# Performance work log

Measured on AMD Instinct MI355X. Metric: run time of the kernel, lower is better.

## Reference

```python
import jax, jax.numpy as jnp
import numpy as np

B, S, H, MI, E, K, SI = 4, 1024, 1024, 512, 16, 2, 2048


def setup_inputs() -> dict:
    key = jax.random.key(0)
    ks = jax.random.split(key, 8)
    s = 0.02  # weight scale ~ glorot-ish
    return {
        "hidden_states": jax.random.normal(ks[0], (B, S, H), jnp.float32),
        "router_w": jax.random.normal(ks[1], (H, E), jnp.float32) * s,
        "expert_gate_up_w": jax.random.normal(ks[2], (E, H, 2 * MI), jnp.float32) * s,
        "expert_down_w": jax.random.normal(ks[3], (E, MI, H), jnp.float32) * s,
        "shared_gate_w": jax.random.normal(ks[4], (H, SI), jnp.float32) * s,
        "shared_up_w": jax.random.normal(ks[5], (H, SI), jnp.float32) * s,
        "shared_down_w": jax.random.normal(ks[6], (SI, H), jnp.float32) * s,
        "shared_expert_gate_w": jax.random.normal(ks[7], (H, 1), jnp.float32) * s,
    }


def reference(hidden_states, router_w, expert_gate_up_w, expert_down_w,
              shared_gate_w, shared_up_w, shared_down_w, shared_expert_gate_w):
    b, s, h = hidden_states.shape
    x = hidden_states.reshape(-1, h)  # [T, H]
    T = x.shape[0]

    # Shared expert: SwiGLU MLP gated by sigmoid(shared_expert_gate)
    g = jax.nn.silu(x @ shared_gate_w)          # [T, SI]
    u = x @ shared_up_w                          # [T, SI]
    shared_out = (u * g) @ shared_down_w         # [T, H]
    shared_out = jax.nn.sigmoid(x @ shared_expert_gate_w) * shared_out

    # Router: softmax -> top-k -> renormalize -> dense [T, E] routing weights
    router_logits = x @ router_w                 # [T, E]
    probs = jax.nn.softmax(router_logits, axis=-1)
    top_p, top_i = jax.lax.top_k(probs, K)       # [T, K]
    top_p = top_p / jnp.sum(top_p, axis=-1, keepdims=True)
    routing = jnp.zeros((T, probs.shape[-1]), x.dtype).at[
        jnp.arange(T)[:, None], top_i].add(top_p)  # [T, E]

    # All-experts SwiGLU (compute-all-then-select, as in source)
    gate_up = jnp.einsum('th,ehm->etm', x, expert_gate_up_w)  # [E, T, 2*MI]
    gate, up = jnp.split(gate_up, 2, axis=-1)
    hidden = up * jax.nn.silu(gate)                            # [E, T, MI]
    expert_out = jnp.einsum('eti,eih->eth', hidden, expert_down_w)  # [E, T, H]
    contrib = jnp.einsum('eth,te->th', expert_out, routing)    # [T, H]

    out = (contrib + shared_out).reshape(b, s, h)
    return out, router_logits
```

## Files before the change

kernel.cpp:

```cpp
#include <hip/hip_runtime.h>
#include <hip/hip_bf16.h>
#include <cstdint>

#define T_  4096
#define H_  1024
#define E_  16
#define MI_ 512
#define SI_ 2048
#define TK_ 8192

typedef __bf16 bf16;
typedef bf16  bf16x8 __attribute__((ext_vector_type(8)));
typedef bf16  bf16x4 __attribute__((ext_vector_type(4)));
typedef float f32x4  __attribute__((ext_vector_type(4)));

__device__ __forceinline__ void gload16(const bf16* g, bf16* lds) {
    __builtin_amdgcn_global_load_lds(
        (const __attribute__((address_space(1))) void*)(uintptr_t)(const void*)g,
        (__attribute__((address_space(3))) void*)(uintptr_t)(void*)lds,
        16, 0, 0);
}

__global__ void k_transpose_all(
    const float* __restrict__ wgu, const float* __restrict__ wdn,
    const float* __restrict__ wsg, const float* __restrict__ wsu, const float* __restrict__ wsd,
    bf16* __restrict__ ogu, bf16* __restrict__ odn,
    bf16* __restrict__ osg, bf16* __restrict__ osu, bf16* __restrict__ osd)
{
    __shared__ float tile[32][33];
    int id = blockIdx.x;
    const float* src; bf16* dst; int R, C, bx, by;
    if (id < 16384) {
        int s = id >> 10, r = id & 1023;
        src = wgu + (size_t)s * 1048576; dst = ogu + (size_t)s * 1048576;
        R = 1024; C = 1024; bx = r & 31; by = r >> 5;
    } else if (id < 24576) {
        int k = id - 16384; int s = k >> 9, r = k & 511;
        src = wdn + (size_t)s * 524288; dst = odn + (size_t)s * 524288;
        R = 512; C = 1024; bx = r & 31; by = r >> 5;
    } else if (id < 26624) {
        int r = id - 24576;
        src = wsg; dst = osg; R = 1024; C = 2048; bx = r & 63; by = r >> 6;
    } else if (id < 28672) {
        int r = id - 26624;
        src = wsu; dst = osu; R = 1024; C = 2048; bx = r & 63; by = r >> 6;
    } else {
        int r = id - 28672;
        src = wsd; dst = osd; R = 2048; C = 1024; bx = r & 31; by = r >> 5;
    }
    int c = bx * 32 + threadIdx.x;
    #pragma unroll
    for (int i = 0; i < 4; i++) {
        int r_ = by * 32 + threadIdx.y + i * 8;
        tile[threadIdx.y + i * 8][threadIdx.x] = src[(size_t)r_ * C + c];
    }
    __syncthreads();
    int rr = by * 32 + threadIdx.x;
    #pragma unroll
    for (int i = 0; i < 4; i++) {
        int cc = bx * 32 + threadIdx.y + i * 8;
        dst[(size_t)cc * R + rr] = (bf16)tile[threadIdx.x][threadIdx.y + i * 8];
    }
}

__global__ __launch_bounds__(256) void k_router(
    const float* __restrict__ x, const float* __restrict__ rw,
    const float* __restrict__ segw, float* __restrict__ logits_out,
    int* __restrict__ top_i, float* __restrict__ top_w,
    float* __restrict__ gate_scalar, bf16* __restrict__ xb)
{
    int wid = threadIdx.x >> 6, lane = threadIdx.x & 63;
    int t = blockIdx.x * 4 + wid;
    const float* xr = x + (size_t)t * H_;
    bf16* xbr = xb + (size_t)t * H_;
    float acc[E_];
    #pragma unroll
    for (int e = 0; e < E_; e++) acc[e] = 0.f;
    float accg = 0.f;
    for (int j = 0; j < H_ / 64; j++) {
        int h = j * 64 + lane;
        float xv = xr[h];
        xbr[h] = (bf16)xv;
        const float4* wrow = reinterpret_cast<const float4*>(rw + (size_t)h * E_);
        #pragma unroll
        for (int q = 0; q < 4; q++) {
            float4 w4 = wrow[q];
            acc[q*4+0] += xv * w4.x; acc[q*4+1] += xv * w4.y;
            acc[q*4+2] += xv * w4.z; acc[q*4+3] += xv * w4.w;
        }
        accg += xv * segw[h];
    }
    #pragma unroll
    for (int off = 32; off >= 1; off >>= 1) {
        #pragma unroll
        for (int e = 0; e < E_; e++) acc[e] += __shfl_xor(acc[e], off);
        accg += __shfl_xor(accg, off);
    }
    if (lane == 0) {
        float* lo = logits_out + (size_t)t * E_;
        #pragma unroll
        for (int e = 0; e < E_; e++) lo[e] = acc[e];
        int i0 = 0; float l0 = acc[0];
        #pragma unroll
        for (int e = 1; e < E_; e++) if (acc[e] > l0) { l0 = acc[e]; i0 = e; }
        int i1 = -1; float l1 = -1e30f;
        #pragma unroll
        for (int e = 0; e < E_; e++) if (e != i0 && acc[e] > l1) { l1 = acc[e]; i1 = e; }
        float w0 = 1.f / (1.f + expf(l1 - l0));
        top_i[t*2] = i0; top_i[t*2+1] = i1;
        top_w[t*2] = w0; top_w[t*2+1] = 1.f - w0;
        gate_scalar[t] = 1.f / (1.f + expf(-accg));
    }
}

__global__ __launch_bounds__(256) void k_count(const int* __restrict__ top_i, int* __restrict__ offsets) {
    __shared__ int hist[256][17];
    int tid = threadIdx.x;
    #pragma unroll
    for (int e = 0; e < E_; e++) hist[tid][e] = 0;
    __syncthreads();
    const int* mine = top_i + tid * 32;
    #pragma unroll
    for (int j = 0; j < 32; j++) hist[tid][mine[j]]++;
    __syncthreads();
    if (tid < E_) {
        int s = 0;
        for (int r = 0; r < 256; r++) s += hist[r][tid];
        hist[0][tid] = s;
    }
    __syncthreads();
    if (tid == 0) {
        int s = 0;
        for (int e = 0; e < E_; e++) { offsets[e] = s; s += hist[0][e]; }
        offsets[E_] = s;
    }
}

__global__ __launch_bounds__(256) void k_fillscan(
    const int* __restrict__ top_i, const int* __restrict__ offsets,
    int* __restrict__ slot_token, int* __restrict__ slot_pos)
{
    int e = blockIdx.x;
    int tid = threadIdx.x;
    int lane = tid & 63, w = tid >> 6;
    __shared__ int wsum[4];

    int t0 = tid * 16;
    unsigned f0 = 0, f1 = 0;
    int c = 0;
    #pragma unroll
    for (int j = 0; j < 16; j++) {
        int t = t0 + j;
        int a = top_i[t*2], b = top_i[t*2+1];
        if (a == e)      { f0 |= 1u << j; c++; }
        else if (b == e) { f1 |= 1u << j; c++; }
    }
    int incl = c;
    #pragma unroll
    for (int off = 1; off < 64; off <<= 1) {
        int v = __shfl_up(incl, off);
        if (lane >= off) incl += v;
    }
    if (lane == 63) wsum[w] = incl;
    __syncthreads();
    int wbase = 0;
    for (int i = 0; i < w; i++) wbase += wsum[i];
    int pos = offsets[e] + wbase + (incl - c);
    #pragma unroll
    for (int j = 0; j < 16; j++) {
        int t = t0 + j;
        if ((f0 >> j) & 1u)      { slot_token[pos] = t; slot_pos[t*2]   = pos; pos++; }
        else if ((f1 >> j) & 1u) { slot_token[pos] = t; slot_pos[t*2+1] = pos; pos++; }
    }
}

__global__ __launch_bounds__(256) void k_mlp1(
    const bf16* __restrict__ xb, const bf16* __restrict__ wgu,
    const bf16* __restrict__ wsg, const bf16* __restrict__ wsu,
    const int* __restrict__ slot_token, const int* __restrict__ offsets,
    bf16* __restrict__ hiddenE, bf16* __restrict__ sh_hid)
{
    int bid = blockIdx.x;
    bool expert = bid < 4096;
    int nt, mt, base, cnt;
    const bf16 *Bg, *Bu;
    bf16* outp; int nout;
    if (expert) {
        int e = bid >> 8; int r = bid & 255; nt = r & 7; mt = r >> 3;
        base = offsets[e]; cnt = offsets[e+1] - base;
        if (mt * 128 >= cnt) return;
        const bf16* wb = wgu + (size_t)e * (2 * MI_) * H_;
        Bg = wb + (size_t)(nt * 64) * H_;
        Bu = wb + (size_t)(MI_ + nt * 64) * H_;
        outp = hiddenE; nout = MI_;
    } else {
        int r = bid - 4096; nt = r & 31; mt = r >> 5;
        base = 0; cnt = T_;
        Bg = wsg + (size_t)(nt * 64) * H_;
        Bu = wsu + (size_t)(nt * 64) * H_;
        outp = sh_hid; nout = SI_;
    }

    __shared__ __align__(16) bf16 As0[128 * 64], Bs0[128 * 64];
    __shared__ __align__(16) bf16 As1[128 * 64], Bs1[128 * 64];

    int tid = threadIdx.x, w = tid >> 6, l = tid & 63;
    int lrow8 = l >> 3;
    int col_off = ((l & 7) ^ lrow8) * 8;

    const bf16* asrc[4];
    const bf16* bsrc[4];
    #pragma unroll
    for (int g = 0; g < 4; g++) {
        int rt = g * 32 + w * 8 + lrow8;
        int s = mt * 128 + rt; if (s >= cnt) s = cnt - 1;
        asrc[g] = (expert ? xb + (size_t)slot_token[base + s] * H_
                          : xb + (size_t)s * H_) + col_off;
        int half = (rt >> 5) & 1;
        int gcol = ((rt >> 6) << 5) | (rt & 31);
        bsrc[g] = (half ? Bu : Bg) + (size_t)gcol * H_ + col_off;
    }

    int lr = l & 15, kq = l >> 4;
    int wm = w & 1, wn = w >> 1;
    f32x4 acc[4][4];
    #pragma unroll
    for (int mi = 0; mi < 4; mi++)
        #pragma unroll
        for (int ni = 0; ni < 4; ni++) acc[mi][ni] = (f32x4){0.f, 0.f, 0.f, 0.f};

    auto STAGE = [&](bf16* Ad, bf16* Bd, int k0) {
        #pragma unroll
        for (int g = 0; g < 4; g++) {
            gload16(asrc[g] + k0, Ad + (g * 32 + w * 8) * 64);
            gload16(bsrc[g] + k0, Bd + (g * 32 + w * 8) * 64);
        }
    };
    auto COMPUTE = [&](const bf16* Ab, const bf16* Bb) {
        #pragma unroll
        for (int ks = 0; ks < 2; ks++) {
            int cl = ((ks * 4 + kq) ^ (lr & 7)) * 8;
            bf16x8 af[4], bfr[4];
            #pragma unroll
            for (int mi = 0; mi < 4; mi++)
                af[mi] = *reinterpret_cast<const bf16x8*>(&Ab[(wm * 64 + mi * 16 + lr) * 64 + cl]);
            #pragma unroll
            for (int ni = 0; ni < 4; ni++)
                bfr[ni] = *reinterpret_cast<const bf16x8*>(&Bb[(wn * 64 + ni * 16 + lr) * 64 + cl]);
            #pragma unroll
            for (int mi = 0; mi < 4; mi++)
                #pragma unroll
                for (int ni = 0; ni < 4; ni++)
                    acc[mi][ni] = __builtin_amdgcn_mfma_f32_16x16x32_bf16(af[mi], bfr[ni], acc[mi][ni], 0, 0, 0);
        }
    };

    STAGE(As0, Bs0, 0);
    __syncthreads();
    for (int k0 = 0; k0 < H_; k0 += 128) {
        STAGE(As1, Bs1, k0 + 64);
        COMPUTE(As0, Bs0);
        __syncthreads();
        if (k0 + 128 < H_) STAGE(As0, Bs0, k0 + 128);
        COMPUTE(As1, Bs1);
        __syncthreads();
    }

    #pragma unroll
    for (int mi = 0; mi < 4; mi++)
        #pragma unroll
        for (int ni = 0; ni < 2; ni++)
            #pragma unroll
            for (int r = 0; r < 4; r++) {
                int row = mt * 128 + wm * 64 + mi * 16 + kq * 4 + r;
                if (row < cnt) {
                    int col = nt * 64 + wn * 32 + ni * 16 + lr;
                    float g = acc[mi][ni][r], u = acc[mi][ni + 2][r];
                    float hv = u * (g / (1.f + expf(-g)));
                    outp[(size_t)(base + row) * nout + col] = (bf16)hv;
                }
            }
}

__global__ __launch_bounds__(256) void k_mlp2(
    const bf16* __restrict__ hiddenE, const bf16* __restrict__ sh_hid,
    const bf16* __restrict__ wdn, const bf16* __restrict__ wsd,
    const int* __restrict__ offsets, const float* __restrict__ gate_s,
    bf16* __restrict__ eo, float* __restrict__ out)
{
    int bid = blockIdx.x;
    bool expert = bid < 4096;
    int nt, mt, base, cnt, KD;
    const bf16 *Ab, *B0;
    if (expert) {
        int e = bid >> 8; int r = bid & 255; nt = r & 7; mt = r >> 3;
        base = offsets[e]; cnt = offsets[e+1] - base;
        if (mt * 128 >= cnt) return;
        KD = MI_;
        Ab = hiddenE;
        B0 = wdn + (size_t)e * H_ * MI_ + (size_t)(nt * 128) * MI_;
    } else {
        int r = bid - 4096; nt = r & 7; mt = r >> 3;
        base = 0; cnt = T_; KD = SI_;
        Ab = sh_hid;
        B0 = wsd + (size_t)(nt * 128) * SI_;
    }

    __shared__ __align__(16) bf16 As0[128 * 64], Bs0[128 * 64];
    __shared__ __align__(16) bf16 As1[128 * 64], Bs1[128 * 64];

    int tid = threadIdx.x, w = tid >> 6, l = tid & 63;
    int lrow8 = l >> 3;
    int col_off = ((l & 7) ^ lrow8) * 8;

    const bf16* asrc[4];
    const bf16* bsrc[4];
    #pragma unroll
    for (int g = 0; g < 4; g++) {
        int rt = g * 32 + w * 8 + lrow8;
        int s = mt * 128 + rt; if (s >= cnt) s = cnt - 1;
        asrc[g] = Ab + (size_t)(base + s) * KD + col_off;
        bsrc[g] = B0 + (size_t)rt * KD + col_off;
    }

    int lr = l & 15, kq = l >> 4;
    int wm = w & 1, wn = w >> 1;
    f32x4 acc[4][4];
    #pragma unroll
    for (int mi = 0; mi < 4; mi++)
        #pragma unroll
        for (int ni = 0; ni < 4; ni++) acc[mi][ni] = (f32x4){0.f, 0.f, 0.f, 0.f};

    auto STAGE = [&](bf16* Ad, bf16* Bd, int k0) {
        #pragma unroll
        for (int g = 0; g < 4; g++) {
            gload16(asrc[g] + k0, Ad + (g * 32 + w * 8) * 64);
            gload16(bsrc[g] + k0, Bd + (g * 32 + w * 8) * 64);
        }
    };
    auto COMPUTE = [&](const bf16* Abuf, const bf16* Bbuf) {
        #pragma unroll
        for (int ks = 0; ks < 2; ks++) {
            int cl = ((ks * 4 + kq) ^ (lr & 7)) * 8;
            bf16x8 af[4], bfr[4];
            #pragma unroll
            for (int mi = 0; mi < 4; mi++)
                af[mi] = *reinterpret_cast<const bf16x8*>(&Abuf[(wm * 64 + mi * 16 + lr) * 64 + cl]);
            #pragma unroll
            for (int ni = 0; ni < 4; ni++)
                bfr[ni] = *reinterpret_cast<const bf16x8*>(&Bbuf[(wn * 64 + ni * 16 + lr) * 64 + cl]);
            #pragma unroll
            for (int mi = 0; mi < 4; mi++)
                #pragma unroll
                for (int ni = 0; ni < 4; ni++)
                    acc[mi][ni] = __builtin_amdgcn_mfma_f32_16x16x32_bf16(af[mi], bfr[ni], acc[mi][ni], 0, 0, 0);
        }
    };

    STAGE(As0, Bs0, 0);
    __syncthreads();
    for (int k0 = 0; k0 < KD; k0 += 128) {
        STAGE(As1, Bs1, k0 + 64);
        COMPUTE(As0, Bs0);
        __syncthreads();
        if (k0 + 128 < KD) STAGE(As0, Bs0, k0 + 128);
        COMPUTE(As1, Bs1);
        __syncthreads();
    }

    #pragma unroll
    for (int mi = 0; mi < 4; mi++)
        #pragma unroll
        for (int ni = 0; ni < 4; ni++)
            #pragma unroll
            for (int r = 0; r < 4; r++) {
                int row = mt * 128 + wm * 64 + mi * 16 + kq * 4 + r;
                if (row < cnt) {
                    int col = nt * 128 + wn * 64 + ni * 16 + lr;
                    float v = acc[mi][ni][r];
                    if (expert) eo[(size_t)(base + row) * H_ + col] = (bf16)v;
                    else        out[(size_t)row * H_ + col] = gate_s[row] * v;
                }
            }
}

__global__ void k_combine(float* __restrict__ out, const bf16* __restrict__ eo,
                          const int* __restrict__ slot_pos, const float* __restrict__ top_w)
{
    int i = blockIdx.x * blockDim.x + threadIdx.x;
    int t = i >> 8;
    int q = (i & 255) * 4;
    int s0 = slot_pos[t*2], s1 = slot_pos[t*2+1];
    float w0 = top_w[t*2], w1 = top_w[t*2+1];
    bf16x4 e0 = *reinterpret_cast<const bf16x4*>(eo + (size_t)s0 * H_ + q);
    bf16x4 e1 = *reinterpret_cast<const bf16x4*>(eo + (size_t)s1 * H_ + q);
    float4* op = reinterpret_cast<float4*>(out) + i;
    float4 so = *op;
    float4 r;
    r.x = so.x + w0 * (float)e0[0] + w1 * (float)e1[0];
    r.y = so.y + w0 * (float)e0[1] + w1 * (float)e1[1];
    r.z = so.z + w0 * (float)e0[2] + w1 * (float)e1[2];
    r.w = so.w + w0 * (float)e0[3] + w1 * (float)e1[3];
    *op = r;
}

extern "C" void kernel_launch(void* const* d_in, const int* in_sizes, int n_in,
                              void* d_out, int out_size, void* d_ws, size_t ws_size,
                              hipStream_t stream) {
    const float* x    = (const float*)d_in[0];
    const float* rw   = (const float*)d_in[1];
    const float* wgu  = (const float*)d_in[2];
    const float* wdn  = (const float*)d_in[3];
    const float* wsg  = (const float*)d_in[4];
    const float* wsu  = (const float*)d_in[5];
    const float* wsd  = (const float*)d_in[6];
    const float* segw = (const float*)d_in[7];
    float* out    = (float*)d_out;
    float* logits = (float*)d_out + (size_t)T_ * H_;

    char* p = (char*)d_ws;
    bf16* xb      = (bf16*)p;  p += (size_t)T_ * H_ * 2;
    bf16* w_guT   = (bf16*)p;  p += (size_t)E_ * H_ * (2*MI_) * 2;
    bf16* w_dnT   = (bf16*)p;  p += (size_t)E_ * MI_ * H_ * 2;
    bf16* w_sgT   = (bf16*)p;  p += (size_t)H_ * SI_ * 2;
    bf16* w_suT   = (bf16*)p;  p += (size_t)H_ * SI_ * 2;
    bf16* w_sdT   = (bf16*)p;  p += (size_t)SI_ * H_ * 2;
    bf16* hiddenE = (bf16*)p;  p += (size_t)TK_ * MI_ * 2;
    bf16* sh_hid  = (bf16*)p;  p += (size_t)T_ * SI_ * 2;
    bf16* eo      = (bf16*)p;  p += (size_t)TK_ * H_ * 2;
    float* gate_s = (float*)p; p += (size_t)T_ * 4;
    int*  top_i   = (int*)p;   p += (size_t)T_ * 2 * 4;
    float* top_w  = (float*)p; p += (size_t)T_ * 2 * 4;
    int*  slot_pos= (int*)p;   p += (size_t)T_ * 2 * 4;
    int*  slot_tok= (int*)p;   p += (size_t)TK_ * 4;
    int*  offsets = (int*)p;   p += 17 * 4;

    k_transpose_all<<<dim3(30720), dim3(32, 8), 0, stream>>>(
        wgu, wdn, wsg, wsu, wsd, w_guT, w_dnT, w_sgT, w_suT, w_sdT);
    k_router<<<dim3(T_/4), 256, 0, stream>>>(x, rw, segw, logits, top_i, top_w, gate_s, xb);
    k_count<<<dim3(1), 256, 0, stream>>>(top_i, offsets);
    k_fillscan<<<dim3(E_), 256, 0, stream>>>(top_i, offsets, slot_tok, slot_pos);

    k_mlp1<<<dim3(4096 + 1024), 256, 0, stream>>>(xb, w_guT, w_sgT, w_suT, slot_tok, offsets, hiddenE, sh_hid);
    k_mlp2<<<dim3(4096 + 256), 256, 0, stream>>>(hiddenE, sh_hid, w_dnT, w_sdT, offsets, gate_s, eo, out);

    k_combine<<<dim3(T_*256/256), 256, 0, stream>>>(out, eo, slot_pos, top_w);
}
```

Baseline: 208.6 us.

## Use fine-grained vmcnt waits in GEMM pipelines and remap blocks across XCDs

Replaces the full __syncthreads barriers in the double-buffered MLP GEMM loops with explicit lgkmcnt/vmcnt waits plus s_barrier. This lets the next stage's global-to-LDS loads stay in flight while the current buffer is computed, instead of draining all memory ops at every barrier. Block indices are also permuted so consecutive hardware blocks, which land on different XCDs, map to contiguous tile ranges and share L2 better. The hand-tuned vmcnt(8) count depends on how many loads STAGE issues, and it risks a race if that count is wrong.

```diff
diff --git a/kernel.cpp b/kernel.cpp
--- a/kernel.cpp
+++ b/kernel.cpp
@@ -20,6 +20,11 @@
         (__attribute__((address_space(3))) void*)(uintptr_t)(void*)lds,
         16, 0, 0);
 }
+
+#define SYNC_LGKM0 do { asm volatile("s_waitcnt lgkmcnt(0)" ::: "memory"); \
+                        __builtin_amdgcn_s_barrier(); } while (0)
+#define SYNC_VM(N) do { asm volatile("s_waitcnt vmcnt(" #N ")" ::: "memory"); \
+                        __builtin_amdgcn_s_barrier(); } while (0)
 
 __global__ void k_transpose_all(
     const float* __restrict__ wgu, const float* __restrict__ wdn,
@@ -180,7 +185,7 @@
     const int* __restrict__ slot_token, const int* __restrict__ offsets,
     bf16* __restrict__ hiddenE, bf16* __restrict__ sh_hid)
 {
-    int bid = blockIdx.x;
+    int bid = (blockIdx.x & 7) * 640 + (blockIdx.x >> 3);
     bool expert = bid < 4096;
     int nt, mt, base, cnt;
     const bf16 *Bg, *Bu;
@@ -256,14 +261,19 @@
     };
 
     STAGE(As0, Bs0, 0);
-    __syncthreads();
     for (int k0 = 0; k0 < H_; k0 += 128) {
+        SYNC_LGKM0;
         STAGE(As1, Bs1, k0 + 64);
+        SYNC_VM(8);
         COMPUTE(As0, Bs0);
-        __syncthreads();
-        if (k0 + 128 < H_) STAGE(As0, Bs0, k0 + 128);
+        SYNC_LGKM0;
+        if (k0 + 128 < H_) {
+            STAGE(As0, Bs0, k0 + 128);
+            SYNC_VM(8);
+        } else {
+            SYNC_VM(0);
+        }
         COMPUTE(As1, Bs1);
-        __syncthreads();
     }
 
     #pragma unroll
@@ -288,7 +298,7 @@
     const int* __restrict__ offsets, const float* __restrict__ gate_s,
     bf16* __restrict__ eo, float* __restrict__ out)
 {
-    int bid = blockIdx.x;
+    int bid = (blockIdx.x & 7) * 544 + (blockIdx.x >> 3);
     bool expert = bid < 4096;
     int nt, mt, base, cnt, KD;
     const bf16 *Ab, *B0;
@@ -358,14 +368,19 @@
     };
 
     STAGE(As0, Bs0, 0);
-    __syncthreads();
     for (int k0 = 0; k0 < KD; k0 += 128) {
+        SYNC_LGKM0;
         STAGE(As1, Bs1, k0 + 64);
+        SYNC_VM(8);
         COMPUTE(As0, Bs0);
-        __syncthreads();
-        if (k0 + 128 < KD) STAGE(As0, Bs0, k0 + 128);
+        SYNC_LGKM0;
+        if (k0 + 128 < KD) {
+            STAGE(As0, Bs0, k0 + 128);
+            SYNC_VM(8);
+        } else {
+            SYNC_VM(0);
+        }
         COMPUTE(As1, Bs1);
-        __syncthreads();
     }
 
     #pragma unroll
```

Result: slower. 411.8 us (+97.4%).
